# Kernel tuning notes

Measured on AMD Instinct MI355X. Metric: run time of the kernel, lower is better.

The kernel has to match this reference:

```python
import jax, jax.numpy as jnp
import numpy as np

SEQ_LEN = 2048
DIM = 1024
HEADS = 16
DIM_HEAD = 64
INNER = HEADS * DIM_HEAD
BASE = 10000.0


def rope_tables(seq_len, head_dim):
    inv_freq = 1.0 / (BASE ** (jnp.arange(0, head_dim, 2, dtype=jnp.float32) / head_dim))
    t = jnp.arange(seq_len, dtype=jnp.float32)
    freqs = jnp.einsum('i,j->ij', t, inv_freq)          # [n, d/2]
    emb = jnp.concatenate([freqs, freqs], axis=-1)       # [n, d]
    return jnp.cos(emb), jnp.sin(emb)                    # each [n, d]


def rotate_half(x):
    d = x.shape[-1] // 2
    return jnp.concatenate([-x[..., d:], x[..., :d]], axis=-1)


def setup_inputs() -> dict:
    key = jax.random.key(0)
    ks = jax.random.split(key, 5)
    x = jax.random.normal(ks[0], (2, SEQ_LEN, DIM), dtype=jnp.float32)
    W_qkv = jax.random.normal(ks[1], (DIM, 3 * INNER), dtype=jnp.float32) * (DIM ** -0.5)
    W_out = jax.random.normal(ks[2], (INNER, DIM), dtype=jnp.float32) * (INNER ** -0.5)
    b_out = jnp.zeros((DIM,), dtype=jnp.float32)
    ln_g = jnp.ones((DIM,), dtype=jnp.float32)
    ln_b = jnp.zeros((DIM,), dtype=jnp.float32)
    return {"x": x, "W_qkv": W_qkv, "W_out": W_out, "b_out": b_out, "ln_g": ln_g, "ln_b": ln_b}


def reference(x, W_qkv, W_out, b_out, ln_g, ln_b):
    b, n, _ = x.shape
    # LayerNorm
    mu = jnp.mean(x, axis=-1, keepdims=True)
    var = jnp.mean(jnp.square(x - mu), axis=-1, keepdims=True)
    xn = (x - mu) * jax.lax.rsqrt(var + 1e-5) * ln_g + ln_b
    # QKV projection -> [b, h, n, d]
    qkv = xn @ W_qkv                                   # [b, n, 3*inner]
    q, k, v = jnp.split(qkv, 3, axis=-1)
    def to_heads(t):
        return t.reshape(b, n, HEADS, DIM_HEAD).transpose(0, 2, 1, 3)
    q, k, v = to_heads(q), to_heads(k), to_heads(v)
    # RoPE
    cos, sin = rope_tables(n, DIM_HEAD)                # [n, d]
    cos = cos[None, None]                              # [1,1,n,d]
    sin = sin[None, None]
    q = q * cos + rotate_half(q) * sin
    k = k * cos + rotate_half(k) * sin
    # Attention
    scale = DIM_HEAD ** -0.5
    dots = jnp.einsum('bhid,bhjd->bhij', q, k) * scale  # [b,h,n,n]
    causal = jnp.tril(jnp.ones((n, n), dtype=bool))
    dots = jnp.where(causal[None, None], dots, jnp.float32(-jnp.inf))
    attn = jax.nn.softmax(dots, axis=-1)
    out = jnp.einsum('bhij,bhjd->bhid', attn, v)       # [b,h,n,d]
    out = out.transpose(0, 2, 1, 3).reshape(b, n, INNER)
    return out @ W_out + b_out
```

## Files before the change

### kernel.cpp

```cpp
#include <hip/hip_runtime.h>
#include <hip/hip_bf16.h>

#define SEQ    2048
#define DMODEL 1024
#define HEADS  16
#define DHEAD  64
#define BATCH  2
#define TOK    (BATCH * SEQ)
#define NQKV   (3 * DMODEL)
#define QK_SCALE (0.125f * 1.4426950408889634f)

typedef __attribute__((ext_vector_type(8))) short bf16x8;
typedef __attribute__((ext_vector_type(4))) float f32x4;

__device__ __forceinline__ float bf2f(ushort u) {
  union { unsigned int i; float f; } v; v.i = ((unsigned int)u) << 16; return v.f;
}
__device__ __forceinline__ ushort f2bf(float f) {
  union { float f; unsigned int i; } v; v.f = f;
  unsigned int r = (v.i + 0x7fffu + ((v.i >> 16) & 1u)) >> 16;
  return (ushort)r;
}

__device__ __forceinline__ int swz(int row, int byteoff) {
  return row * 128 + (byteoff ^ ((row & 7) << 4));
}
__device__ __forceinline__ int kperm(int s) {
  return (s & 0x20) | ((s & 0x0C) << 1) | ((s & 0x10) >> 2) | (s & 3);
}

#define GLL16(g, l)                                                                     \
  __builtin_amdgcn_global_load_lds((const __attribute__((address_space(1))) void*)(g),  \
                                   (__attribute__((address_space(3))) void*)(l), 16, 0, 0)

__global__ __launch_bounds__(256) void ln_kernel(const float* __restrict__ x,
                                                 const float* __restrict__ g,
                                                 const float* __restrict__ b,
                                                 ushort* __restrict__ xn) {
  int t = blockIdx.x;
  int tid = threadIdx.x;
  const float* row = x + (size_t)t * DMODEL;
  float4 v = *(const float4*)(row + tid * 4);
  float s  = v.x + v.y + v.z + v.w;
  float s2 = v.x * v.x + v.y * v.y + v.z * v.z + v.w * v.w;
#pragma unroll
  for (int m = 32; m >= 1; m >>= 1) {
    s  += __shfl_down(s, m);
    s2 += __shfl_down(s2, m);
  }
  __shared__ float ws[4], ws2[4];
  if ((tid & 63) == 0) { ws[tid >> 6] = s; ws2[tid >> 6] = s2; }
  __syncthreads();
  s  = ws[0] + ws[1] + ws[2] + ws[3];
  s2 = ws2[0] + ws2[1] + ws2[2] + ws2[3];
  float mu  = s * (1.f / DMODEL);
  float var = s2 * (1.f / DMODEL) - mu * mu;
  float rs  = rsqrtf(var + 1e-5f);
  float4 gv = *(const float4*)(g + tid * 4);
  float4 bv = *(const float4*)(b + tid * 4);
  ushort4 o;
  o.x = f2bf((v.x - mu) * rs * gv.x + bv.x);
  o.y = f2bf((v.y - mu) * rs * gv.y + bv.y);
  o.z = f2bf((v.z - mu) * rs * gv.z + bv.z);
  o.w = f2bf((v.w - mu) * rs * gv.w + bv.w);
  *(ushort4*)(xn + (size_t)t * DMODEL + tid * 4) = o;
}

__global__ void transpose_f2b(const float* __restrict__ in, ushort* __restrict__ out,
                              int R, int C) {
  __shared__ float tile[32][33];
  int c0 = blockIdx.x * 32, r0 = blockIdx.y * 32;
  int x = threadIdx.x, y = threadIdx.y;
#pragma unroll
  for (int i = 0; i < 32; i += 8) tile[y + i][x] = in[(size_t)(r0 + y + i) * C + c0 + x];
  __syncthreads();
#pragma unroll
  for (int i = 0; i < 32; i += 8) out[(size_t)(c0 + y + i) * R + r0 + x] = f2bf(tile[x][y + i]);
}

__global__ void rope_tab_kernel(float* __restrict__ ct, float* __restrict__ st) {
  int n = blockIdx.x, d = threadIdx.x;
  float invf = expf(-logf(10000.f) * (float)(d & 31) * (1.f / 32.f));
  float a = (float)n * invf;
  ct[n * DHEAD + d] = cosf(a);
  st[n * DHEAD + d] = sinf(a);
}

template<int EPI>
__global__ __launch_bounds__(256) void gemm_bt(const ushort* __restrict__ A,
                                               const ushort* __restrict__ BT,
                                               float* __restrict__ Cf,
                                               const float* __restrict__ bias,
                                               ushort* __restrict__ qh,
                                               ushort* __restrict__ kh,
                                               ushort* __restrict__ vh,
                                               const float* __restrict__ ct,
                                               const float* __restrict__ st,
                                               int M, int N, int K) {
  __shared__ __align__(16) ushort As[128 * 32];
  __shared__ __align__(16) ushort Bs[128 * 32];
  int tid = threadIdx.x;
  int w = tid >> 6, lane = tid & 63;
  int lrow = lane & 15, g = lane >> 4, lk = g << 3;
  int m0 = blockIdx.y * 128, n0 = blockIdx.x * 128;
  int wr = (w >> 1) * 64, wc = (w & 1) * 64;
  int grow = lane >> 2, gcol = (lane & 3) * 8;
  ushort* ldsA0 = As + w * 512;
  ushort* ldsA1 = As + 2048 + w * 512;
  ushort* ldsB0 = Bs + w * 512;
  ushort* ldsB1 = Bs + 2048 + w * 512;
  f32x4 acc[4][4] = {};
  for (int k0 = 0; k0 < K; k0 += 32) {
    __syncthreads();
    GLL16(A  + (size_t)(m0 + w * 16 + grow) * K + k0 + gcol, ldsA0);
    GLL16(A  + (size_t)(m0 + 64 + w * 16 + grow) * K + k0 + gcol, ldsA1);
    GLL16(BT + (size_t)(n0 + w * 16 + grow) * K + k0 + gcol, ldsB0);
    GLL16(BT + (size_t)(n0 + 64 + w * 16 + grow) * K + k0 + gcol, ldsB1);
    __syncthreads();
    bf16x8 af[4], bfr[4];
#pragma unroll
    for (int i = 0; i < 4; i++) af[i]  = *(const bf16x8*)(As + (wr + i * 16 + lrow) * 32 + lk);
#pragma unroll
    for (int i = 0; i < 4; i++) bfr[i] = *(const bf16x8*)(Bs + (wc + i * 16 + lrow) * 32 + lk);
    __builtin_amdgcn_s_setprio(1);
#pragma unroll
    for (int mf = 0; mf < 4; mf++)
#pragma unroll
      for (int nf = 0; nf < 4; nf++)
        acc[mf][nf] = __builtin_amdgcn_mfma_f32_16x16x32_bf16(af[mf], bfr[nf], acc[mf][nf], 0, 0, 0);
    __builtin_amdgcn_s_setprio(0);
  }
#pragma unroll
  for (int mf = 0; mf < 4; mf++)
#pragma unroll
    for (int nf = 0; nf < 4; nf++) {
      int col = n0 + wc + nf * 16 + lrow;
#pragma unroll
      for (int r = 0; r < 4; r++) {
        int rowi = m0 + wr + mf * 16 + g * 4 + r;
        float val = acc[mf][nf][r];
        if (EPI == 2) {
          Cf[(size_t)rowi * N + col] = val + bias[col];
        } else {
          int mat = col >> 10, c1 = col & 1023;
          int h = c1 >> 6, d = c1 & 63;
          int bb = rowi >> 11, n = rowi & (SEQ - 1);
          if (mat < 2) {
            float partner = acc[mf][nf ^ 2][r];
            float cs = ct[n * DHEAD + d], sn = st[n * DHEAD + d];
            float sgn = (d & 32) ? 1.f : -1.f;
            val = val * cs + sgn * partner * sn;
            if (mat == 0) val *= QK_SCALE;
          }
          ushort* dst = (mat == 0) ? qh : (mat == 1) ? kh : vh;
          dst[((size_t)(bb * HEADS + h) * SEQ + n) * DHEAD + d] = f2bf(val);
        }
      }
    }
}

__global__ __launch_bounds__(256) void attn_kernel(const ushort* __restrict__ q,
                                                   const ushort* __restrict__ k,
                                                   const ushort* __restrict__ v,
                                                   ushort* __restrict__ ao) {
  int wgid = blockIdx.x + gridDim.x * blockIdx.y;
  int j5 = wgid >> 3;
  int bh  = (wgid & 7) * 4 + (j5 >> 4);
  int pid = j5 & 15;
  int qlo = pid, qhi = (SEQ / 64 - 1) - pid;
  int tid = threadIdx.x, w = tid >> 6, lane = tid & 63;
  int lrow = lane & 15, g = lane >> 4;
  __shared__ __align__(16) ushort Ks[2][64 * 64];
  __shared__ __align__(16) ushort Vt[2][64 * 64];
  const ushort* qb = q + (size_t)bh * SEQ * DHEAD;
  const ushort* kb = k + (size_t)bh * SEQ * DHEAD;
  const ushort* vb = v + (size_t)bh * SEQ * DHEAD;
  const ushort* qph = qb + (size_t)(qhi * 64 + w * 16 + lrow) * DHEAD + g * 8;
  const ushort* qpl = qb + (size_t)(qlo * 64 + w * 16 + lrow) * DHEAD + g * 8;
  bf16x8 qh0 = *(const bf16x8*)(qph), qh1 = *(const bf16x8*)(qph + 32);
  bf16x8 ql0 = *(const bf16x8*)(qpl), ql1 = *(const bf16x8*)(qpl + 32);
  f32x4 aOh[4] = {}, aOl[4] = {};
  float l_hi = 0.f, l_lo = 0.f;

  int krow = tid >> 2, kco = (tid & 3) * 16;
  int pik = kperm(krow);
  int d0 = (tid & 31) * 2, kv8 = (tid >> 5) * 8;
  int4 ka0, ka1;
  unsigned int vd[8];

#define STAGE_ISSUE(j)                                                          \
  {                                                                             \
    const ushort* ks = kb + ((size_t)((j) * 64 + pik)) * DHEAD + kco;           \
    ka0 = *(const int4*)ks;                                                     \
    ka1 = *(const int4*)(ks + 8);                                               \
    const ushort* vs = vb + ((size_t)((j) * 64 + kv8)) * DHEAD + d0;            \
    _Pragma("unroll")                                                           \
    for (int jj = 0; jj < 8; jj++) vd[jj] = *(const unsigned int*)(vs + jj * DHEAD); \
  }

#define STAGE_WRITE(bsel)                                                       \
  {                                                                             \
    char* kd = (char*)Ks[bsel];                                                 \
    *(int4*)(kd + swz(krow, (tid & 3) * 32)) = ka0;                             \
    *(int4*)(kd + swz(krow, (tid & 3) * 32 + 16)) = ka1;                        \
    unsigned int lo[4], hi[4];                                                  \
    _Pragma("unroll")                                                           \
    for (int jj = 0; jj < 4; jj++) {                                            \
      lo[jj] = __builtin_amdgcn_perm(vd[2 * jj + 1], vd[2 * jj], 0x05040100u);  \
      hi[jj] = __builtin_amdgcn_perm(vd[2 * jj + 1], vd[2 * jj], 0x07060302u);  \
    }                                                                           \
    char* vdst = (char*)Vt[bsel];                                               \
    *(int4*)(vdst + swz(d0, kv8 * 2))     = *(int4*)lo;                         \
    *(int4*)(vdst + swz(d0 + 1, kv8 * 2)) = *(int4*)hi;                         \
  }

  STAGE_ISSUE(0);
  STAGE_WRITE(0);
  __syncthreads();
  int cur = 0;

  for (int jt = 0; jt <= qhi; jt++) {
    if (jt < qhi) STAGE_ISSUE(jt + 1);
    const char* kbuf = (const char*)Ks[cur];
    const char* vbuf = (const char*)Vt[cur];
    bf16x8 kf[8];
#pragma unroll
    for (int nf = 0; nf < 4; nf++) {
      kf[2 * nf]     = *(const bf16x8*)(kbuf + swz(nf * 16 + lrow, g * 16));
      kf[2 * nf + 1] = *(const bf16x8*)(kbuf + swz(nf * 16 + lrow, g * 16 + 64));
    }
    bf16x8 pah0, pah1, pal0, pal1;
    bool do_lo = (jt <= qlo);
    {
      f32x4 aS[4] = {};
      __builtin_amdgcn_s_setprio(1);
#pragma unroll
      for (int nf = 0; nf < 4; nf++) {
        aS[nf] = __builtin_amdgcn_mfma_f32_16x16x32_bf16(kf[2 * nf], qh0, aS[nf], 0, 0, 0);
        aS[nf] = __builtin_amdgcn_mfma_f32_16x16x32_bf16(kf[2 * nf + 1], qh1, aS[nf], 0, 0, 0);
      }
      __builtin_amdgcn_s_setprio(0);
      union { bf16x8 v; ushort u[8]; } a0, a1;
      bool diag = (jt == qhi);
#pragma unroll
      for (int nf = 0; nf < 4; nf++)
#pragma unroll
        for (int r = 0; r < 4; r++) {
          int kvl = (nf >> 1) * 32 + g * 8 + (nf & 1) * 4 + r;
          float p = exp2f(aS[nf][r]);
          if (diag && kvl > w * 16 + lrow) p = 0.f;
          l_hi += p;
          ushort pb = f2bf(p);
          if (nf < 2) a0.u[(nf & 1) * 4 + r] = pb;
          else        a1.u[(nf & 1) * 4 + r] = pb;
        }
      pah0 = a0.v; pah1 = a1.v;
    }
    if (do_lo) {
      f32x4 aS[4] = {};
      __builtin_amdgcn_s_setprio(1);
#pragma unroll
      for (int nf = 0; nf < 4; nf++) {
        aS[nf] = __builtin_amdgcn_mfma_f32_16x16x32_bf16(kf[2 * nf], ql0, aS[nf], 0, 0, 0);
        aS[nf] = __builtin_amdgcn_mfma_f32_16x16x32_bf16(kf[2 * nf + 1], ql1, aS[nf], 0, 0, 0);
      }
      __builtin_amdgcn_s_setprio(0);
      union { bf16x8 v; ushort u[8]; } a0, a1;
      bool diag = (jt == qlo);
#pragma unroll
      for (int nf = 0; nf < 4; nf++)
#pragma unroll
        for (int r = 0; r < 4; r++) {
          int kvl = (nf >> 1) * 32 + g * 8 + (nf & 1) * 4 + r;
          float p = exp2f(aS[nf][r]);
          if (diag && kvl > w * 16 + lrow) p = 0.f;
          l_lo += p;
          ushort pb = f2bf(p);
          if (nf < 2) a0.u[(nf & 1) * 4 + r] = pb;
          else        a1.u[(nf & 1) * 4 + r] = pb;
        }
      pal0 = a0.v; pal1 = a1.v;
    }
    bf16x8 vf[8];
#pragma unroll
    for (int nf = 0; nf < 4; nf++) {
      vf[2 * nf]     = *(const bf16x8*)(vbuf + swz(nf * 16 + lrow, g * 16));
      vf[2 * nf + 1] = *(const bf16x8*)(vbuf + swz(nf * 16 + lrow, g * 16 + 64));
    }
    __builtin_amdgcn_s_setprio(1);
#pragma unroll
    for (int nf = 0; nf < 4; nf++) {
      aOh[nf] = __builtin_amdgcn_mfma_f32_16x16x32_bf16(pah0, vf[2 * nf], aOh[nf], 0, 0, 0);
      aOh[nf] = __builtin_amdgcn_mfma_f32_16x16x32_bf16(pah1, vf[2 * nf + 1], aOh[nf], 0, 0, 0);
    }
    if (do_lo) {
#pragma unroll
      for (int nf = 0; nf < 4; nf++) {
        aOl[nf] = __builtin_amdgcn_mfma_f32_16x16x32_bf16(pal0, vf[2 * nf], aOl[nf], 0, 0, 0);
        aOl[nf] = __builtin_amdgcn_mfma_f32_16x16x32_bf16(pal1, vf[2 * nf + 1], aOl[nf], 0, 0, 0);
      }
    }
    __builtin_amdgcn_s_setprio(0);
    if (jt < qhi) STAGE_WRITE(cur ^ 1);
    __syncthreads();
    cur ^= 1;
  }

  l_hi += __shfl_xor(l_hi, 16); l_hi += __shfl_xor(l_hi, 32);
  l_lo += __shfl_xor(l_lo, 16); l_lo += __shfl_xor(l_lo, 32);
  int b = bh >> 4, h = bh & 15;
#pragma unroll
  for (int r = 0; r < 4; r++) {
    float ih = 1.f / __shfl(l_hi, g * 4 + r);
    float il = 1.f / __shfl(l_lo, g * 4 + r);
#pragma unroll
    for (int nf = 0; nf < 4; nf++) {
      int col = h * DHEAD + nf * 16 + lrow;
      int th = b * SEQ + qhi * 64 + w * 16 + g * 4 + r;
      int tl = b * SEQ + qlo * 64 + w * 16 + g * 4 + r;
      ao[(size_t)th * DMODEL + col] = f2bf(aOh[nf][r] * ih);
      ao[(size_t)tl * DMODEL + col] = f2bf(aOl[nf][r] * il);
    }
  }
#undef STAGE_ISSUE
#undef STAGE_WRITE
}

extern "C" void kernel_launch(void* const* d_in, const int* in_sizes, int n_in,
                              void* d_out, int out_size, void* d_ws, size_t ws_size,
                              hipStream_t stream) {
  const float* x    = (const float*)d_in[0];
  const float* Wqkv = (const float*)d_in[1];
  const float* Wout = (const float*)d_in[2];
  const float* bout = (const float*)d_in[3];
  const float* lng  = (const float*)d_in[4];
  const float* lnb  = (const float*)d_in[5];
  float* out = (float*)d_out;

  ushort* xn    = (ushort*)d_ws;
  ushort* WqkvT = xn + (size_t)TOK * DMODEL;
  ushort* WoutT = WqkvT + (size_t)NQKV * DMODEL;
  ushort* qh    = WoutT + (size_t)DMODEL * DMODEL;
  ushort* kh    = qh + (size_t)BATCH * HEADS * SEQ * DHEAD;
  ushort* vh    = kh + (size_t)BATCH * HEADS * SEQ * DHEAD;
  float*  ct    = (float*)(vh + (size_t)BATCH * HEADS * SEQ * DHEAD);
  float*  st    = ct + SEQ * DHEAD;
  ushort* ao    = xn;

  hipLaunchKernelGGL(ln_kernel, dim3(TOK), dim3(256), 0, stream, x, lng, lnb, xn);
  hipLaunchKernelGGL(transpose_f2b, dim3(NQKV / 32, DMODEL / 32), dim3(32, 8), 0, stream,
                     Wqkv, WqkvT, DMODEL, NQKV);
  hipLaunchKernelGGL(transpose_f2b, dim3(DMODEL / 32, DMODEL / 32), dim3(32, 8), 0, stream,
                     Wout, WoutT, DMODEL, DMODEL);
  hipLaunchKernelGGL(rope_tab_kernel, dim3(SEQ), dim3(DHEAD), 0, stream, ct, st);
  hipLaunchKernelGGL(gemm_bt<1>, dim3(NQKV / 128, TOK / 128), dim3(256), 0, stream,
                     xn, WqkvT, (float*)nullptr, (const float*)nullptr,
                     qh, kh, vh, ct, st, TOK, NQKV, DMODEL);
  hipLaunchKernelGGL(attn_kernel, dim3(16, BATCH * HEADS), dim3(256), 0, stream,
                     qh, kh, vh, ao);
  hipLaunchKernelGGL(gemm_bt<2>, dim3(DMODEL / 128, TOK / 128), dim3(256), 0, stream,
                     ao, WoutT, out, bout,
                     (ushort*)nullptr, (ushort*)nullptr, (ushort*)nullptr,
                     (const float*)nullptr, (const float*)nullptr, TOK, DMODEL, DMODEL);
}
```

Baseline: 138.0 us.

## Double GEMM K-tile with swizzled LDS, XCD-aware block remap, packed bf16 conversion

The QKV/out GEMM now stages 64-wide K slices per iteration instead of 32. This halves the number of barrier pairs, and the LDS is XOR-swizzled to avoid bank conflicts on fragment reads. Workgroup IDs are remapped in groups of 8 so neighbouring tiles land on the same XCD for better L2 reuse. In attention, the softmax probabilities are converted to bf16 with the packed float2-to-bfloat162 intrinsic instead of a manual rounding routine. LDS use doubles, which can reduce occupancy.

Result: slower. 146.9 us (+6.4%).

```diff
diff --git a/kernel.cpp b/kernel.cpp
--- a/kernel.cpp
+++ b/kernel.cpp
@@ -97,38 +97,48 @@
                                                const float* __restrict__ ct,
                                                const float* __restrict__ st,
                                                int M, int N, int K) {
-  __shared__ __align__(16) ushort As[128 * 32];
-  __shared__ __align__(16) ushort Bs[128 * 32];
+  __shared__ __align__(16) ushort As[128 * 64];
+  __shared__ __align__(16) ushort Bs[128 * 64];
   int tid = threadIdx.x;
   int w = tid >> 6, lane = tid & 63;
-  int lrow = lane & 15, g = lane >> 4, lk = g << 3;
-  int m0 = blockIdx.y * 128, n0 = blockIdx.x * 128;
+  int lrow = lane & 15, g = lane >> 4;
+  int gx = gridDim.x;
+  int wg = blockIdx.x + gx * blockIdx.y;
+  int nwg = gx * gridDim.y;
+  int cpx = nwg >> 3;
+  int swg = (wg & 7) * cpx + (wg >> 3);
+  int m0 = (swg / gx) * 128, n0 = (swg % gx) * 128;
   int wr = (w >> 1) * 64, wc = (w & 1) * 64;
-  int grow = lane >> 2, gcol = (lane & 3) * 8;
-  ushort* ldsA0 = As + w * 512;
-  ushort* ldsA1 = As + 2048 + w * 512;
-  ushort* ldsB0 = Bs + w * 512;
-  ushort* ldsB1 = Bs + 2048 + w * 512;
+  int r8 = lane >> 3, s8 = lane & 7;
+  int scol = (s8 ^ r8) * 8;
   f32x4 acc[4][4] = {};
-  for (int k0 = 0; k0 < K; k0 += 32) {
+  for (int k0 = 0; k0 < K; k0 += 64) {
     __syncthreads();
-    GLL16(A  + (size_t)(m0 + w * 16 + grow) * K + k0 + gcol, ldsA0);
-    GLL16(A  + (size_t)(m0 + 64 + w * 16 + grow) * K + k0 + gcol, ldsA1);
-    GLL16(BT + (size_t)(n0 + w * 16 + grow) * K + k0 + gcol, ldsB0);
-    GLL16(BT + (size_t)(n0 + 64 + w * 16 + grow) * K + k0 + gcol, ldsB1);
+#pragma unroll
+    for (int c = 0; c < 4; c++) {
+      int row = w * 32 + c * 8;
+      GLL16(A  + (size_t)(m0 + row + r8) * K + k0 + scol, As + row * 64);
+      GLL16(BT + (size_t)(n0 + row + r8) * K + k0 + scol, Bs + row * 64);
+    }
     __syncthreads();
-    bf16x8 af[4], bfr[4];
-#pragma unroll
-    for (int i = 0; i < 4; i++) af[i]  = *(const bf16x8*)(As + (wr + i * 16 + lrow) * 32 + lk);
-#pragma unroll
-    for (int i = 0; i < 4; i++) bfr[i] = *(const bf16x8*)(Bs + (wc + i * 16 + lrow) * 32 + lk);
-    __builtin_amdgcn_s_setprio(1);
-#pragma unroll
-    for (int mf = 0; mf < 4; mf++)
-#pragma unroll
-      for (int nf = 0; nf < 4; nf++)
-        acc[mf][nf] = __builtin_amdgcn_mfma_f32_16x16x32_bf16(af[mf], bfr[nf], acc[mf][nf], 0, 0, 0);
-    __builtin_amdgcn_s_setprio(0);
+#pragma unroll
+    for (int ks = 0; ks < 2; ks++) {
+      bf16x8 af[4], bf[4];
+#pragma unroll
+      for (int i = 0; i < 4; i++) {
+        int ra = wr + i * 16 + lrow;
+        af[i] = *(const bf16x8*)((const char*)As + swz(ra, g * 16 + ks * 64));
+        int rb = wc + i * 16 + lrow;
+        bf[i] = *(const bf16x8*)((const char*)Bs + swz(rb, g * 16 + ks * 64));
+      }
+      __builtin_amdgcn_s_setprio(1);
+#pragma unroll
+      for (int mf = 0; mf < 4; mf++)
+#pragma unroll
+        for (int nf = 0; nf < 4; nf++)
+          acc[mf][nf] = __builtin_amdgcn_mfma_f32_16x16x32_bf16(af[mf], bf[nf], acc[mf][nf], 0, 0, 0);
+      __builtin_amdgcn_s_setprio(0);
+    }
   }
 #pragma unroll
   for (int mf = 0; mf < 4; mf++)
@@ -240,20 +250,23 @@
         aS[nf] = __builtin_amdgcn_mfma_f32_16x16x32_bf16(kf[2 * nf + 1], qh1, aS[nf], 0, 0, 0);
       }
       __builtin_amdgcn_s_setprio(0);
-      union { bf16x8 v; ushort u[8]; } a0, a1;
+      union { bf16x8 v; __hip_bfloat162 h[4]; } a0, a1;
       bool diag = (jt == qhi);
 #pragma unroll
-      for (int nf = 0; nf < 4; nf++)
+      for (int nf = 0; nf < 4; nf++) {
+        float p[4];
 #pragma unroll
         for (int r = 0; r < 4; r++) {
           int kvl = (nf >> 1) * 32 + g * 8 + (nf & 1) * 4 + r;
-          float p = exp2f(aS[nf][r]);
-          if (diag && kvl > w * 16 + lrow) p = 0.f;
-          l_hi += p;
-          ushort pb = f2bf(p);
-          if (nf < 2) a0.u[(nf & 1) * 4 + r] = pb;
-          else        a1.u[(nf & 1) * 4 + r] = pb;
+          p[r] = exp2f(aS[nf][r]);
+          if (diag && kvl > w * 16 + lrow) p[r] = 0.f;
+          l_hi += p[r];
         }
+        __hip_bfloat162 plo = __float22bfloat162_rn({p[0], p[1]});
+        __hip_bfloat162 phi = __float22bfloat162_rn({p[2], p[3]});
+        if (nf < 2) { a0.h[(nf & 1) * 2] = plo; a0.h[(nf & 1) * 2 + 1] = phi; }
+        else        { a1.h[(nf & 1) * 2] = plo; a1.h[(nf & 1) * 2 + 1] = phi; }
+      }
       pah0 = a0.v; pah1 = a1.v;
     }
     if (do_lo) {
@@ -265,20 +278,23 @@
         aS[nf] = __builtin_amdgcn_mfma_f32_16x16x32_bf16(kf[2 * nf + 1], ql1, aS[nf], 0, 0, 0);
       }
       __builtin_amdgcn_s_setprio(0);
-      union { bf16x8 v; ushort u[8]; } a0, a1;
+      union { bf16x8 v; __hip_bfloat162 h[4]; } a0, a1;
       bool diag = (jt == qlo);
 #pragma unroll
-      for (int nf = 0; nf < 4; nf++)
+      for (int nf = 0; nf < 4; nf++) {
+        float p[4];
 #pragma unroll
         for (int r = 0; r < 4; r++) {
           int kvl = (nf >> 1) * 32 + g * 8 + (nf & 1) * 4 + r;
-          float p = exp2f(aS[nf][r]);
-          if (diag && kvl > w * 16 + lrow) p = 0.f;
-          l_lo += p;
-          ushort pb = f2bf(p);
-          if (nf < 2) a0.u[(nf & 1) * 4 + r] = pb;
-          else        a1.u[(nf & 1) * 4 + r] = pb;
+          p[r] = exp2f(aS[nf][r]);
+          if (diag && kvl > w * 16 + lrow) p[r] = 0.f;
+          l_lo += p[r];
         }
+        __hip_bfloat162 plo = __float22bfloat162_rn({p[0], p[1]});
+        __hip_bfloat162 phi = __float22bfloat162_rn({p[2], p[3]});
+        if (nf < 2) { a0.h[(nf & 1) * 2] = plo; a0.h[(nf & 1) * 2 + 1] = phi; }
+        else        { a1.h[(nf & 1) * 2] = plo; a1.h[(nf & 1) * 2 + 1] = phi; }
+      }
       pal0 = a0.v; pal1 = a1.v;
     }
     bf16x8 vf[8];
```
